# Kernel tuning notes

Measured on AMD Instinct MI355X. Metric: run time of the kernel, lower is better.

Reference implementation:

```python
import jax, jax.numpy as jnp
import numpy as np

HEADS, DHEAD = 4, 64            # TransformerConv heads / out_channels
MAX_EDGE_DIST = 1.0

def _ln(x, g, b):
    m = jnp.mean(x, -1, keepdims=True)
    v = jnp.mean((x - m) ** 2, -1, keepdims=True)
    return (x - m) * jax.lax.rsqrt(v + 1e-5) * g + b


def _embed_conv(node_feat, entity_type, adjv, mask, emb, W1, b1, g1, be1, Wh, bh, gh, beh):
    # aggr='add' message passing over dense masked adjacency. mask[b,s,t]: edge s->t.
    B, N, _ = mask.shape
    src = jnp.concatenate([node_feat, emb[entity_type]], -1)          # [B,N,F+E]
    msg = jnp.concatenate(
        [jnp.broadcast_to(src[:, :, None, :], (B, N, N, src.shape[-1])),
         adjv[..., None]], -1)                                        # [B,Ns,Nt,F+E+1]
    h = _ln(jax.nn.relu(msg @ W1 + b1), g1, be1)                      # lin1
    h = _ln(jax.nn.relu(h @ Wh + bh), gh, beh)                        # lin2[0]
    return jnp.einsum('bst,bsth->bth', mask, h)                       # sum over sources


def _tconv(x, adjv, mask, Wq, bq, Wk, bk, Wv, bv, We, Ws, bs):
    # PyG TransformerConv (beta=False, dropout=0, root_weight=True, concat=True).
    B, N, _ = x.shape
    q = (x @ Wq + bq).reshape(B, N, HEADS, DHEAD)
    k = (x @ Wk + bk).reshape(B, N, HEADS, DHEAD)
    v = (x @ Wv + bv).reshape(B, N, HEADS, DHEAD)
    we = We.reshape(HEADS, DHEAD)                                     # edge_dim=1, no bias
    scale = 1.0 / jnp.sqrt(jnp.asarray(DHEAD, x.dtype))
    # score[b,h,s,t] = q_t . (k_s + adjv[s,t]*we) * scale
    qk = jnp.einsum('bshd,bthd->bhst', k, q)
    qe = jnp.einsum('bthd,hd->bht', q, we)
    logits = (qk + adjv[:, None, :, :] * qe[:, :, None, :]) * scale
    mh = mask[:, None, :, :]                                          # [B,1,Ns,Nt]
    masked = jnp.where(mh > 0, logits, -1e30)
    mmax = jnp.max(masked, axis=2, keepdims=True)
    w = jnp.exp(masked - mmax) * mh
    den = jnp.sum(w, axis=2, keepdims=True)
    alpha = w / jnp.maximum(den, 1e-16)                               # softmax over sources per target
    out = jnp.einsum('bhst,bshd->bthd', alpha, v)
    out = out + jnp.einsum('bhst,bst->bth', alpha, adjv)[..., None] * we
    out = out.reshape(B, N, HEADS * DHEAD)
    return out + x @ Ws + bs                                          # skip (root) connection


def _forward(node_feat, entity_type, adj, agent_id, emb, W1, b1, g1, be1, Wh, bh, gh, beh,
             Wq1, bq1, Wk1, bk1, Wv1, bv1, We1, Ws1, bs1,
             Wq2, bq2, Wk2, bk2, Wv2, bv2, We2, Ws2, bs2):
    mask = ((adj > 0) & (adj < MAX_EDGE_DIST)).astype(adj.dtype)
    adjv = adj * mask
    x = _embed_conv(node_feat, entity_type, adjv, mask, emb, W1, b1, g1, be1, Wh, bh, gh, beh)
    x = jax.nn.relu(_tconv(x, adjv, mask, Wq1, bq1, Wk1, bk1, Wv1, bv1, We1, Ws1, bs1))
    x = jax.nn.relu(_tconv(x, adjv, mask, Wq2, bq2, Wk2, bk2, Wv2, bv2, We2, Ws2, bs2))
    return x[jnp.arange(x.shape[0]), agent_id]                        # gather agent node feats


def setup_inputs() -> dict:
    key = jax.random.key(0)
    ks = jax.random.split(key, 24)
    B, N, F, E, H = 32, 128, 9, 8, 128
    HD = HEADS * DHEAD
    s = 0.05
    p = lambda k, shape: (jax.random.normal(k, shape, jnp.float32) * s)
    inp = {
        'node_feat': jax.random.normal(ks[0], (B, N, F), jnp.float32),
        'entity_type': jax.random.randint(ks[1], (B, N), 0, 8),
        'adj': jax.random.uniform(ks[2], (B, N, N), jnp.float32, 0.0, 2.0),
        'agent_id': jax.random.randint(ks[3], (B,), 0, N),
        'emb': p(ks[4], (8, E)),
        'W1': p(ks[5], (F + E + 1, H)), 'b1': jnp.zeros(H), 'g1': jnp.ones(H), 'be1': jnp.zeros(H),
        'Wh': p(ks[6], (H, H)), 'bh': jnp.zeros(H), 'gh': jnp.ones(H), 'beh': jnp.zeros(H),
        'Wq1': p(ks[7], (H, HD)), 'bq1': jnp.zeros(HD),
        'Wk1': p(ks[8], (H, HD)), 'bk1': jnp.zeros(HD),
        'Wv1': p(ks[9], (H, HD)), 'bv1': jnp.zeros(HD),
        'We1': p(ks[10], (1, HD)),
        'Ws1': p(ks[11], (H, HD)), 'bs1': jnp.zeros(HD),
        'Wq2': p(ks[12], (HD, HD)), 'bq2': jnp.zeros(HD),
        'Wk2': p(ks[13], (HD, HD)), 'bk2': jnp.zeros(HD),
        'Wv2': p(ks[14], (HD, HD)), 'bv2': jnp.zeros(HD),
        'We2': p(ks[15], (1, HD)),
        'Ws2': p(ks[16], (HD, HD)), 'bs2': jnp.zeros(HD),
    }
    return inp


def reference(node_feat, entity_type, adj, agent_id, emb, W1, b1, g1, be1, Wh, bh, gh, beh,
              Wq1, bq1, Wk1, bk1, Wv1, bv1, We1, Ws1, bs1,
              Wq2, bq2, Wk2, bk2, Wv2, bv2, We2, Ws2, bs2):
    return _forward(node_feat, entity_type, adj, agent_id, emb, W1, b1, g1, be1, Wh, bh, gh, beh,
                    Wq1, bq1, Wk1, bk1, Wv1, bv1, We1, Ws1, bs1,
                    Wq2, bq2, Wk2, bk2, Wv2, bv2, We2, Ws2, bs2)
```

## Files before the change

### kernel.cpp

```cpp
#include <hip/hip_runtime.h>
#include <hip/hip_bf16.h>

typedef __hip_bfloat16 bf16;
typedef unsigned short ushort_t;
typedef unsigned char uchar_t;
typedef unsigned int uint_t;
typedef __attribute__((ext_vector_type(8))) short short8;
typedef __attribute__((ext_vector_type(4))) float fx4;
typedef __attribute__((ext_vector_type(4))) unsigned int uintx4;

#define BB 32
#define NN 128
#define FF 9
#define EE 8
#define HH 128
#define HD 256
#define NHEAD 4
#define DHEAD 64

__device__ __forceinline__ float us2f(ushort_t u) {
    return __uint_as_float(((unsigned int)u) << 16);
}
__device__ __forceinline__ ushort_t f2us_tr(float f) {
    return (ushort_t)(__float_as_uint(f) >> 16);
}
__device__ __forceinline__ short8 pack4(uint_t w0, uint_t w1, uint_t w2, uint_t w3) {
    uintx4 u = (uintx4){w0, w1, w2, w3};
    return __builtin_bit_cast(short8, u);
}
__device__ __forceinline__ void pair_split(float a, float c, uint_t& hw, uint_t& lw) {
    uint_t ua = __float_as_uint(a), uc = __float_as_uint(c);
    uint_t ka = ua & 0xffff0000u, kc = uc & 0xffff0000u;
    float la = a - __uint_as_float(ka);
    float lc = c - __uint_as_float(kc);
    hw = (ua >> 16) | kc;
    lw = (__float_as_uint(la) >> 16) | (__float_as_uint(lc) & 0xffff0000u);
}
__device__ __forceinline__ uint_t pair_hi(float a, float c) {
    return (__float_as_uint(a) >> 16) | (__float_as_uint(c) & 0xffff0000u);
}

__global__ void TransformerConvNet_85315230367963_kernel() {}

__global__ void k_sent(float* out, float val) {
    out[blockIdx.x * 256 + threadIdx.x] = val;
}

__global__ void __launch_bounds__(256) k_prep_all(
    const float* adj, float* adjvT, uchar_t* sl_s, float* sl_av, int* cnts,
    int* tmapG,
    const float* nf, const int* et, const float* emb, const float* W1,
    const float* b1, float* base, float* x0,
    const float* Wh, const float* g1, const float* be1, const float* bh,
    ushort_t* BhiG, ushort_t* BloG, float* W1s, float* cbv,
    const float* Wq1, const float* Wk1, const float* Wv1, const float* Ws1,
    ushort_t* WhA, ushort_t* WlA,
    const float* Wq2, const float* Wk2, const float* Wv2, const float* Ws2,
    ushort_t* WhB, ushort_t* WlB)
{
    __shared__ float tileF[128 * 33];
    __shared__ int   cntL[256];

    int blk = blockIdx.x;
    int tid = threadIdx.x;

    if (blk < 32) {
        int b = blk;
        int wv = tid >> 6, lane = tid & 63;
        for (int c = 0; c < 4; c++) {
            int t0c = c * 32;
#pragma unroll
            for (int pass = 0; pass < 16; pass++) {
                int s = pass * 8 + (tid >> 5);
                int tq = tid & 31;
                float a = adj[(b * NN + s) * NN + t0c + tq];
                float av = (a > 0.f && a < 1.0f) ? a : 0.f;
                tileF[s * 33 + tq] = av;
            }
            __syncthreads();
#pragma unroll
            for (int j = 0; j < 16; j++) {
                int u = wv * 16 + j;
                int tq = u >> 1, sh = u & 1;
                int t = t0c + tq;
                int s = sh * 64 + lane;
                float av = tileF[s * 33 + tq];
                adjvT[(b * NN + t) * NN + s] = av;
                unsigned long long mask = __ballot(av != 0.f);
                int key = (b * NN + t) * 2 + sh;
                if (av != 0.f) {
                    int pos = __popcll(mask & ((1ull << lane) - 1ull));
                    sl_s[key * 64 + pos] = (uchar_t)s;
                    sl_av[key * 64 + pos] = av;
                }
                if (lane == 0) {
                    int cv = (int)__popcll(mask);
                    cnts[key] = cv;
                    cntL[t * 2 + sh] = cv;
                    if (mask == 0ull) { sl_s[key * 64] = 0; sl_av[key * 64] = 0.f; }
                }
            }
            __syncthreads();
        }
        {
            int sh = tid >> 7, i = tid & 127;
            int ci = cntL[i * 2 + sh];
            int rank = 0;
            for (int j = 0; j < 128; j++) {
                int cj = cntL[j * 2 + sh];
                rank += (cj > ci) || (cj == ci && j < i);
            }
            tmapG[b * 256 + sh * 128 + rank] = i;
        }
    } else if (blk < 1056) {
        int bblk = blk - 32;
        int c = tid & 127;
#pragma unroll
        for (int rr = 0; rr < 2; rr++) {
            int bs = bblk * 4 + rr * 2 + (tid >> 7);
            int ty = et[bs];
            float acc = b1[c];
            for (int f = 0; f < FF; f++)
                acc += nf[bs * FF + f] * W1[f * HH + c];
            for (int e2 = 0; e2 < EE; e2++)
                acc += emb[ty * EE + e2] * W1[(FF + e2) * HH + c];
            base[bs * HH + c] = acc;
        }
    } else if (blk < 1312) {
        int zblk = blk - 1056;
        float4* p = (float4*)x0 + zblk * 512 + tid * 2;
        p[0] = (float4){0.f, 0.f, 0.f, 0.f};
        p[1] = (float4){0.f, 0.f, 0.f, 0.f};
    } else if (blk < 1344) {
        int n = (blk - 1312) * 4 + (tid >> 6);
        int t = tid & 63;
        int sw = 8 * (n & 15);
        float s1 = 0.f, s2 = 0.f;
#pragma unroll
        for (int kk = 0; kk < 2; kk++) {
            int k = t + kk * 64;
            float w = Wh[k * HH + n];
            float wp = g1[k] * w;
            ushort_t hb = f2us_tr(wp);
            float lo = wp - us2f(hb);
            BhiG[n * HH + (k ^ sw)] = hb;
            BloG[n * HH + (k ^ sw)] = f2us_tr(lo);
            s1 += wp;
            s2 += be1[k] * w;
        }
        for (int m = 1; m < 64; m <<= 1) {
            s1 += __shfl_xor(s1, m);
            s2 += __shfl_xor(s2, m);
        }
        if (t == 0) { W1s[n] = s1; cbv[n] = s2 + bh[n]; }
    } else if (blk < 1600) {
        int key = (blk - 1344) * 4 + (tid >> 6);
        int lane = tid & 63;
        int mat = key >> 8, n = key & 255;
        const float* W = (mat == 0) ? Wq1 : (mat == 1) ? Wk1 : (mat == 2) ? Wv1 : Ws1;
        ushort_t* hi = WhA + mat * 256 * HH;
        ushort_t* lo = WlA + mat * 256 * HH;
        int sw = 8 * (n & 15);
        for (int k = lane; k < HH; k += 64) {
            float w = W[k * HD + n];
            ushort_t hb = f2us_tr(w);
            float l = w - us2f(hb);
            hi[n * HH + (k ^ sw)] = hb;
            lo[n * HH + (k ^ sw)] = f2us_tr(l);
        }
    } else {
        int key = (blk - 1600) * 4 + (tid >> 6);
        int lane = tid & 63;
        int mat = key >> 8, n = key & 255;
        const float* W = (mat == 0) ? Wq2 : (mat == 1) ? Wk2 : (mat == 2) ? Wv2 : Ws2;
        ushort_t* hi = WhB + mat * 256 * HD;
        ushort_t* lo = WlB + mat * 256 * HD;
        int sw = 8 * (n & 15);
        for (int k = lane; k < HD; k += 64) {
            float w = W[k * HD + n];
            ushort_t hb = f2us_tr(w);
            float l = w - us2f(hb);
            hi[n * HD + (k ^ sw)] = hb;
            lo[n * HD + (k ^ sw)] = f2us_tr(l);
        }
    }
}

__global__ void __launch_bounds__(256) k_econv_mfma(
    const uchar_t* sl_s, const float* sl_av, const int* cnts, const int* tmapG,
    const float* base, const float* W1,
    const ushort_t* BhiG, const ushort_t* BloG,
    const float* W1sg, const float* cbv,
    const float* ghp, const float* behp, float* x0)
{
    __shared__ __align__(16) ushort_t PhiPlo[2 * HH * HH];
    __shared__ int tmap16[16];
    ushort_t* Phi = PhiPlo;
    ushort_t* Plo = PhiPlo + HH * HH;

    int blk = blockIdx.x;
    int b  = blk >> 4;
    int tt = (blk >> 1) & 7;
    int sh = blk & 1;
    if (b >= BB / 2) tt = 7 - tt;
    int t0 = tt * 16;
    int tid = threadIdx.x;
    int wv  = tid >> 6;
    int lane = tid & 63;
    int nl = lane & 15;
    int quad = lane >> 4;

    if (tid < 16) tmap16[tid] = tmapG[b * 256 + sh * 128 + t0 + tid];

    {
        const uint4* srcH = (const uint4*)BhiG;
        const uint4* srcL = (const uint4*)BloG;
        uint4* dstH = (uint4*)Phi;
        uint4* dstL = (uint4*)Plo;
        for (int i = tid; i < HH * HH / 8; i += 256) {
            dstH[i] = srcH[i];
            dstL[i] = srcL[i];
        }
    }

    float w17v[4][8];
#pragma unroll
    for (int st = 0; st < 4; st++) {
        const float* p = W1 + 17 * HH + quad * 8 + 32 * st;
        float4 a = *(const float4*)p;
        float4 bq = *(const float4*)(p + 4);
        w17v[st][0] = a.x;  w17v[st][1] = a.y;  w17v[st][2] = a.z;  w17v[st][3] = a.w;
        w17v[st][4] = bq.x; w17v[st][5] = bq.y; w17v[st][6] = bq.z; w17v[st][7] = bq.w;
    }

    __syncthreads();

    int myt = tmap16[nl];
    int key = ((b << 7) + myt) * 2 + sh;
    int cnt = cnts[key];
    int q = (cnt + 3) >> 2;
    int mq = q;
#pragma unroll
    for (int m = 1; m < 16; m <<= 1) mq = max(mq, __shfl_xor(mq, m));
    const uchar_t* lst_s = sl_s + key * 64;
    const float*   lst_a = sl_av + key * 64;
    int i0 = wv * q;

    fx4 acc1[8];
#pragma unroll
    for (int tile = 0; tile < 8; tile++) acc1[tile] = (fx4){0.f, 0.f, 0.f, 0.f};
    float c0 = 0.f;
    float c1 = 0.f;

    for (int i = 0; i < mq; i++) {
        int idx = i0 + i;
        bool val = (i < q) && (idx < cnt);
        int ridx = (idx < cnt) ? idx : (cnt > 0 ? cnt - 1 : 0);
        int s = lst_s[ridx];
        float avv = val ? lst_a[ridx] : 0.f;
        const float* brow = base + (b * NN + s) * HH;

        short8 Hhi[4], Hlo[4];
        float sm = 0.f, s2 = 0.f;
#pragma unroll
        for (int st = 0; st < 4; st++) {
            const float* p = brow + quad * 8 + 32 * st;
            float4 b0 = *(const float4*)p;
            float4 b1q = *(const float4*)(p + 4);
            float h[8] = {b0.x, b0.y, b0.z, b0.w, b1q.x, b1q.y, b1q.z, b1q.w};
            uint_t hw[4], lw[4];
#pragma unroll
            for (int pr = 0; pr < 4; pr++) {
                float a = fmaxf(fmaf(avv, w17v[st][2 * pr], h[2 * pr]), 0.f);
                float c = fmaxf(fmaf(avv, w17v[st][2 * pr + 1], h[2 * pr + 1]), 0.f);
                sm += a; sm += c;
                s2 = fmaf(a, a, s2);
                s2 = fmaf(c, c, s2);
                pair_split(a, c, hw[pr], lw[pr]);
            }
            Hhi[st] = pack4(hw[0], hw[1], hw[2], hw[3]);
            Hlo[st] = pack4(lw[0], lw[1], lw[2], lw[3]);
        }
        sm += __shfl_xor(sm, 16); sm += __shfl_xor(sm, 32);
        s2 += __shfl_xor(s2, 16); s2 += __shfl_xor(s2, 32);
        float m1 = sm * (1.f / 128.f);
        float r1 = rsqrtf(s2 * (1.f / 128.f) - m1 * m1 + 1e-5f);
        float nm = -m1 * r1;

        fx4 G[8];
#pragma unroll
        for (int tile = 0; tile < 8; tile++) G[tile] = (fx4){0.f, 0.f, 0.f, 0.f};
#pragma unroll
        for (int st = 0; st < 4; st++) {
            int koff = quad * 8 + 32 * st;
#pragma unroll
            for (int tile = 0; tile < 8; tile++) {
                int off = (tile * 16 + nl) * HH + (koff ^ (nl * 8));
                short8 ph = *(const short8*)(&Phi[off]);
                short8 pl = *(const short8*)(&Plo[off]);
                G[tile] = __builtin_amdgcn_mfma_f32_16x16x32_bf16(ph, Hhi[st], G[tile], 0, 0, 0);
                G[tile] = __builtin_amdgcn_mfma_f32_16x16x32_bf16(pl, Hhi[st], G[tile], 0, 0, 0);
                G[tile] = __builtin_amdgcn_mfma_f32_16x16x32_bf16(ph, Hlo[st], G[tile], 0, 0, 0);
            }
        }

        float sm2 = 0.f, ss2 = 0.f;
#pragma unroll
        for (int tile = 0; tile < 8; tile++) {
            float4 w4 = *(const float4*)(W1sg + tile * 16 + quad * 4);
            float4 c4 = *(const float4*)(cbv + tile * 16 + quad * 4);
            float wa[4] = {w4.x, w4.y, w4.z, w4.w};
            float ca[4] = {c4.x, c4.y, c4.z, c4.w};
#pragma unroll
            for (int r = 0; r < 4; r++) {
                float pre = fmaf(r1, G[tile][r], fmaf(nm, wa[r], ca[r]));
                float h2 = fmaxf(pre, 0.f);
                G[tile][r] = h2;
                sm2 += h2;
                ss2 = fmaf(h2, h2, ss2);
            }
        }
        sm2 += __shfl_xor(sm2, 16); sm2 += __shfl_xor(sm2, 32);
        ss2 += __shfl_xor(ss2, 16); ss2 += __shfl_xor(ss2, 32);
        float mean2 = sm2 * (1.f / 128.f);
        float r2 = rsqrtf(ss2 * (1.f / 128.f) - mean2 * mean2 + 1e-5f);
        float msk = val ? 1.f : 0.f;
        float mr2 = msk * r2;

#pragma unroll
        for (int tile = 0; tile < 8; tile++)
#pragma unroll
            for (int r = 0; r < 4; r++)
                acc1[tile][r] = fmaf(mr2, G[tile][r], acc1[tile][r]);
        c0 += msk;
        c1 = fmaf(mr2, mean2, c1);
    }

    __syncthreads();
    float* slab = (float*)PhiPlo;
#pragma unroll
    for (int tile = 0; tile < 8; tile++) {
        float4 g4 = *(const float4*)(ghp + tile * 16 + quad * 4);
        float4 be4 = *(const float4*)(behp + tile * 16 + quad * 4);
        float gv[4] = {g4.x, g4.y, g4.z, g4.w};
        float bv[4] = {be4.x, be4.y, be4.z, be4.w};
#pragma unroll
        for (int r = 0; r < 4; r++) {
            float xv = fmaf(gv[r], acc1[tile][r] - c1, bv[r] * c0);
            slab[(wv * 16 + nl) * 132 + tile * 16 + quad * 4 + r] = xv;
        }
    }
    __syncthreads();
    for (int e = tid; e < 16 * HH; e += 256) {
        int t = e >> 7, n = e & 127;
        float vsum = slab[t * 132 + n] + slab[(16 + t) * 132 + n]
                   + slab[(32 + t) * 132 + n] + slab[(48 + t) * 132 + n];
        atomicAdd(&x0[(b * NN + tmap16[t]) * HH + n], vsum);
    }
}

template <int IN>
__global__ void __launch_bounds__(256) k_qkvs_mfma(
    const float* x, const ushort_t* Whi, const ushort_t* Wlo,
    const float* b0, const float* b1, const float* b2, const float* b3,
    float* q, float* skipo,
    ushort_t* khi, ushort_t* klo, ushort_t* vThi, ushort_t* vTlo,
    const int* agentp)
{
    const int ST = IN / 32;
    int blk = blockIdx.x;
    int m0 = (blk >> 3) * 64;
    int nsl = blk & 7;
    int tid = threadIdx.x;
    int wv = tid >> 6;
    int lane = tid & 63;
    int nl = lane & 15;
    int quad = lane >> 4;
    int row = m0 + wv * 16 + nl;

    short8 Ahi[ST], Alo[ST];
    const float* xrow = x + (long)row * IN;
#pragma unroll
    for (int st = 0; st < ST; st++) {
        const float* p = xrow + quad * 8 + 32 * st;
        float4 a4 = *(const float4*)p;
        float4 b4 = *(const float4*)(p + 4);
        float h[8] = {a4.x, a4.y, a4.z, a4.w, b4.x, b4.y, b4.z, b4.w};
        uint_t hw[4], lw[4];
#pragma unroll
        for (int pr = 0; pr < 4; pr++)
            pair_split(h[2 * pr], h[2 * pr + 1], hw[pr], lw[pr]);
        Ahi[st] = pack4(hw[0], hw[1], hw[2], hw[3]);
        Alo[st] = pack4(lw[0], lw[1], lw[2], lw[3]);
    }

    const float* bs_[4] = {b0, b1, b2, b3};
    int rw0 = m0 + wv * 16;
    bool agset = (agentp != nullptr);
    int agrow = agset ? agentp[rw0 >> 7] : -1;
    bool havea = agset && ((agrow >> 4) == ((rw0 & 127) >> 4));

#pragma unroll
    for (int mat = 0; mat < 4; mat++) {
        if ((mat == 0 || mat == 3) && agset && !havea) continue;
        const ushort_t* Bh = Whi + (mat * 256 + nsl * 32) * IN;
        const ushort_t* Bl = Wlo + (mat * 256 + nsl * 32) * IN;
        fx4 G[2];
#pragma unroll
        for (int tile = 0; tile < 2; tile++) {
            float bc = bs_[mat][nsl * 32 + tile * 16 + nl];
            G[tile] = (fx4){bc, bc, bc, bc};
        }
#pragma unroll
        for (int st = 0; st < ST; st++) {
            int koff = quad * 8 + 32 * st;
#pragma unroll
            for (int tile = 0; tile < 2; tile++) {
                int off = (tile * 16 + nl) * IN + (koff ^ (nl * 8));
                short8 bh8 = *(const short8*)(Bh + off);
                short8 bl8 = *(const short8*)(Bl + off);
                G[tile] = __builtin_amdgcn_mfma_f32_16x16x32_bf16(Ahi[st], bh8, G[tile], 0, 0, 0);
                G[tile] = __builtin_amdgcn_mfma_f32_16x16x32_bf16(Alo[st], bh8, G[tile], 0, 0, 0);
                G[tile] = __builtin_amdgcn_mfma_f32_16x16x32_bf16(Ahi[st], bl8, G[tile], 0, 0, 0);
            }
        }
        int row0 = m0 + wv * 16 + quad * 4;
        if (mat == 0 || mat == 3) {
            float* om = (mat == 0) ? q : skipo;
#pragma unroll
            for (int tile = 0; tile < 2; tile++)
#pragma unroll
                for (int r = 0; r < 4; r++)
                    om[(row0 + r) * HD + nsl * 32 + tile * 16 + nl] = G[tile][r];
        } else if (mat == 1) {
#pragma unroll
            for (int tile = 0; tile < 2; tile++) {
                int col = nsl * 32 + tile * 16 + nl;
#pragma unroll
                for (int r = 0; r < 4; r++) {
                    float gv = G[tile][r];
                    ushort_t hb = f2us_tr(gv);
                    khi[(row0 + r) * HD + col] = hb;
                    klo[(row0 + r) * HD + col] = f2us_tr(gv - us2f(hb));
                }
            }
        } else {
            int bb = row0 >> 7;
            int s0 = row0 & 127;
#pragma unroll
            for (int tile = 0; tile < 2; tile++) {
                int col = nsl * 32 + tile * 16 + nl;
                int dg = bb * 256 + col;
                ushort4 h4, l4;
                float g0 = G[tile][0], g1 = G[tile][1], g2 = G[tile][2], g3 = G[tile][3];
                ushort_t h0 = f2us_tr(g0), h1 = f2us_tr(g1), h2 = f2us_tr(g2), h3 = f2us_tr(g3);
                h4.x = h0; h4.y = h1; h4.z = h2; h4.w = h3;
                l4.x = f2us_tr(g0 - us2f(h0));
                l4.y = f2us_tr(g1 - us2f(h1));
                l4.z = f2us_tr(g2 - us2f(h2));
                l4.w = f2us_tr(g3 - us2f(h3));
                *(ushort4*)&vThi[dg * NN + s0] = h4;
                *(ushort4*)&vTlo[dg * NN + s0] = l4;
            }
        }
    }
}

__global__ void __launch_bounds__(128) k_attn_mfma(
    const float* qb, const ushort_t* khi, const ushort_t* klo,
    const ushort_t* vThi, const ushort_t* vTlo,
    const float* adjvT, const float* We, const float* skip, float* xout,
    const int* agentp, float* outp)
{
    __shared__ float aL[16][132];
    __shared__ float qeL[16];
    __shared__ float mxL[2][16];
    __shared__ float dnL[2][16];
    __shared__ float ebL[2][16];

    int blk = blockIdx.x;
    int b, h, tt;
    if (agentp == nullptr) {
        b = blk >> 5; h = (blk >> 3) & 3; tt = blk & 7;
    } else {
        b = blk >> 2; h = blk & 3; tt = agentp[b] >> 4;
    }
    int t0 = tt * 16;
    int tid = threadIdx.x;
    int w   = tid >> 6;
    int lane = tid & 63;
    int nl = lane & 15;
    int quad = lane >> 4;

    short8 Qhi[2], Qlo[2];
    float qe = 0.f;
#pragma unroll
    for (int ks = 0; ks < 2; ks++) {
        const float* p = qb + (b * NN + t0 + nl) * HD + h * DHEAD + quad * 8 + 32 * ks;
        const float* wp = We + h * DHEAD + quad * 8 + 32 * ks;
        float4 a0 = *(const float4*)p;
        float4 a1 = *(const float4*)(p + 4);
        float4 w0 = *(const float4*)wp;
        float4 w1 = *(const float4*)(wp + 4);
        float hv[8] = {a0.x, a0.y, a0.z, a0.w, a1.x, a1.y, a1.z, a1.w};
        float wv8[8] = {w0.x, w0.y, w0.z, w0.w, w1.x, w1.y, w1.z, w1.w};
        uint_t hw[4], lw[4];
#pragma unroll
        for (int pr = 0; pr < 4; pr++) {
            float a = hv[2 * pr], c = hv[2 * pr + 1];
            qe = fmaf(a, wv8[2 * pr], qe);
            qe = fmaf(c, wv8[2 * pr + 1], qe);
            pair_split(a, c, hw[pr], lw[pr]);
        }
        Qhi[ks] = pack4(hw[0], hw[1], hw[2], hw[3]);
        Qlo[ks] = pack4(lw[0], lw[1], lw[2], lw[3]);
    }
    qe += __shfl_xor(qe, 16);
    qe += __shfl_xor(qe, 32);
    if (w == 0 && lane < 16) qeL[lane] = qe;
    __syncthreads();
    float qe_r[4];
#pragma unroll
    for (int r = 0; r < 4; r++) qe_r[r] = qeL[quad * 4 + r];
    float we_d[2];
#pragma unroll
    for (int nt2 = 0; nt2 < 2; nt2++) we_d[nt2] = We[h * DHEAD + (w * 2 + nt2) * 16 + nl];

    fx4 S[4];
#pragma unroll
    for (int st = 0; st < 4; st++) S[st] = (fx4){0.f, 0.f, 0.f, 0.f};
#pragma unroll
    for (int ks = 0; ks < 2; ks++) {
#pragma unroll
        for (int st = 0; st < 4; st++) {
            long off = (long)(b * NN + (w * 4 + st) * 16 + nl) * HD + h * DHEAD + quad * 8 + 32 * ks;
            short8 bh8 = *(const short8*)(khi + off);
            short8 bl8 = *(const short8*)(klo + off);
            S[st] = __builtin_amdgcn_mfma_f32_16x16x32_bf16(Qhi[ks], bh8, S[st], 0, 0, 0);
            S[st] = __builtin_amdgcn_mfma_f32_16x16x32_bf16(Qlo[ks], bh8, S[st], 0, 0, 0);
            S[st] = __builtin_amdgcn_mfma_f32_16x16x32_bf16(Qhi[ks], bl8, S[st], 0, 0, 0);
        }
    }

    float av[4][4];
#pragma unroll
    for (int st = 0; st < 4; st++)
#pragma unroll
        for (int r = 0; r < 4; r++)
            av[st][r] = adjvT[(b * NN + t0 + quad * 4 + r) * NN + (w * 4 + st) * 16 + nl];
#pragma unroll
    for (int st = 0; st < 4; st++)
#pragma unroll
        for (int r = 0; r < 4; r++) {
            float a = av[st][r];
            S[st][r] = (a != 0.f) ? (S[st][r] + a * qe_r[r]) * 0.125f : -1e30f;
        }

    float mxp[4];
#pragma unroll
    for (int r = 0; r < 4; r++) {
        float m = S[0][r];
#pragma unroll
        for (int st = 1; st < 4; st++) m = fmaxf(m, S[st][r]);
#pragma unroll
        for (int mm = 1; mm < 16; mm <<= 1) m = fmaxf(m, __shfl_xor(m, mm));
        mxp[r] = m;
    }
    if (nl == 0) {
#pragma unroll
        for (int r = 0; r < 4; r++) mxL[w][quad * 4 + r] = mxp[r];
    }
    __syncthreads();
    float mx[4];
#pragma unroll
    for (int r = 0; r < 4; r++)
        mx[r] = fmaxf(mxL[0][quad * 4 + r], mxL[1][quad * 4 + r]);

    float dnp[4] = {0.f, 0.f, 0.f, 0.f}, ebp[4] = {0.f, 0.f, 0.f, 0.f};
#pragma unroll
    for (int st = 0; st < 4; st++)
#pragma unroll
        for (int r = 0; r < 4; r++) {
            float e = (av[st][r] != 0.f) ? __expf(S[st][r] - mx[r]) : 0.f;
            S[st][r] = e;
            dnp[r] += e;
            ebp[r] = fmaf(e, av[st][r], ebp[r]);
        }
#pragma unroll
    for (int r = 0; r < 4; r++) {
#pragma unroll
        for (int mm = 1; mm < 16; mm <<= 1) {
            dnp[r] += __shfl_xor(dnp[r], mm);
            ebp[r] += __shfl_xor(ebp[r], mm);
        }
    }
    if (nl == 0) {
#pragma unroll
        for (int r = 0; r < 4; r++) {
            dnL[w][quad * 4 + r] = dnp[r];
            ebL[w][quad * 4 + r] = ebp[r];
        }
    }
    __syncthreads();
    float rden[4], beta[4];
#pragma unroll
    for (int r = 0; r < 4; r++) {
        int row = quad * 4 + r;
        float d = dnL[0][row] + dnL[1][row];
        rden[r] = 1.f / fmaxf(d, 1e-16f);
        beta[r] = (ebL[0][row] + ebL[1][row]) * rden[r];
    }

#pragma unroll
    for (int st = 0; st < 4; st++)
#pragma unroll
        for (int r = 0; r < 4; r++)
            aL[quad * 4 + r][(w * 4 + st) * 16 + nl] = S[st][r] * rden[r];
    __syncthreads();

    short8 Ah[4];
#pragma unroll
    for (int ks = 0; ks < 4; ks++) {
        const float* p = &aL[nl][quad * 8 + 32 * ks];
        float4 a0 = *(const float4*)p;
        float4 a1 = *(const float4*)(p + 4);
        float hv[8] = {a0.x, a0.y, a0.z, a0.w, a1.x, a1.y, a1.z, a1.w};
        uint_t ww[4];
#pragma unroll
        for (int pr = 0; pr < 4; pr++) ww[pr] = pair_hi(hv[2 * pr], hv[2 * pr + 1]);
        Ah[ks] = pack4(ww[0], ww[1], ww[2], ww[3]);
    }

    fx4 G[2];
#pragma unroll
    for (int nt2 = 0; nt2 < 2; nt2++) {
        fx4 g;
#pragma unroll
        for (int r = 0; r < 4; r++) g[r] = beta[r] * we_d[nt2];
        G[nt2] = g;
    }
#pragma unroll
    for (int ks = 0; ks < 4; ks++) {
#pragma unroll
        for (int nt2 = 0; nt2 < 2; nt2++) {
            long dg = (long)(b * 256 + h * DHEAD + (w * 2 + nt2) * 16 + nl);
            const short8 vh = *(const short8*)(vThi + dg * NN + quad * 8 + 32 * ks);
            const short8 vl = *(const short8*)(vTlo + dg * NN + quad * 8 + 32 * ks);
            G[nt2] = __builtin_amdgcn_mfma_f32_16x16x32_bf16(Ah[ks], vh, G[nt2], 0, 0, 0);
            G[nt2] = __builtin_amdgcn_mfma_f32_16x16x32_bf16(Ah[ks], vl, G[nt2], 0, 0, 0);
        }
    }

    if (agentp == nullptr) {
#pragma unroll
        for (int nt2 = 0; nt2 < 2; nt2++)
#pragma unroll
            for (int r = 0; r < 4; r++) {
                int gi = (b * NN + t0 + quad * 4 + r) * HD + h * DHEAD + (w * 2 + nt2) * 16 + nl;
                xout[gi] = fmaxf(G[nt2][r] + skip[gi], 0.f);
            }
    } else {
        int ag = agentp[b];
#pragma unroll
        for (int nt2 = 0; nt2 < 2; nt2++)
#pragma unroll
            for (int r = 0; r < 4; r++) {
                int t = t0 + quad * 4 + r;
                if (t == ag) {
                    int d = h * DHEAD + (w * 2 + nt2) * 16 + nl;
                    int gi = (b * NN + t) * HD + d;
                    outp[b * HD + d] = fmaxf(G[nt2][r] + skip[gi], 0.f);
                }
            }
    }
}

extern "C" void kernel_launch(void* const* d_in, const int* in_sizes, int n_in,
                              void* d_out, int out_size, void* d_ws, size_t ws_size,
                              hipStream_t stream) {
    float* out = (float*)d_out;
    (void)hipGetLastError();

    bool ok = (n_in == 31) && in_sizes[0] == BB * NN * FF && in_sizes[2] == BB * NN * NN
              && in_sizes[5] == (FF + EE + 1) * HH && in_sizes[13] == HH * HD
              && in_sizes[22] == HD * HD && out_size == BB * HD;
    if (!ok) { k_sent<<<32, 256, 0, stream>>>(out, -30000.f); return; }

    const size_t WS_NEED = (size_t)8912896 * 4;
    if (ws_size < WS_NEED) { k_sent<<<32, 256, 0, stream>>>(out, -20000.f); return; }

    const float* nf    = (const float*)d_in[0];
    const int*   et    = (const int*)d_in[1];
    const float* adj   = (const float*)d_in[2];
    const int*   agent = (const int*)d_in[3];
    const float* emb   = (const float*)d_in[4];
    const float* W1    = (const float*)d_in[5];
    const float* b1    = (const float*)d_in[6];
    const float* g1    = (const float*)d_in[7];
    const float* be1   = (const float*)d_in[8];
    const float* Wh    = (const float*)d_in[9];
    const float* bh    = (const float*)d_in[10];
    const float* gh    = (const float*)d_in[11];
    const float* beh   = (const float*)d_in[12];
    const float* Wq1   = (const float*)d_in[13];
    const float* bq1   = (const float*)d_in[14];
    const float* Wk1   = (const float*)d_in[15];
    const float* bk1   = (const float*)d_in[16];
    const float* Wv1   = (const float*)d_in[17];
    const float* bv1   = (const float*)d_in[18];
    const float* We1   = (const float*)d_in[19];
    const float* Ws1   = (const float*)d_in[20];
    const float* bs1   = (const float*)d_in[21];
    const float* Wq2   = (const float*)d_in[22];
    const float* bq2   = (const float*)d_in[23];
    const float* Wk2   = (const float*)d_in[24];
    const float* bk2   = (const float*)d_in[25];
    const float* Wv2   = (const float*)d_in[26];
    const float* bv2   = (const float*)d_in[27];
    const float* We2   = (const float*)d_in[28];
    const float* Ws2   = (const float*)d_in[29];
    const float* bs2   = (const float*)d_in[30];

    float* ws   = (float*)d_ws;
    float* slav = ws;
    float* base = ws + 524288;
    float* x0   = base + BB * NN * HH;
    float* q    = x0 + BB * NN * HH;
    float* kreg = q + BB * NN * HD;
    float* vreg = kreg + BB * NN * HD;
    float* skip = vreg + BB * NN * HD;
    float* areg = skip + BB * NN * HD;
    float* x1   = areg + BB * NN * HD;
    float* x2   = x1 + BB * NN * HD;

    ushort_t* BhiG = (ushort_t*)q;
    ushort_t* BloG = BhiG + HH * HH;
    float*    W1sW = q + 16384;
    float*    cbW  = q + 16512;
    int*      cnts = (int*)(q + 17024);
    int*      tmapG = (int*)(q + 25216);

    ushort_t* khi  = (ushort_t*)kreg;
    ushort_t* klo  = khi + BB * NN * HD;
    ushort_t* vThi = (ushort_t*)vreg;
    ushort_t* vTlo = vThi + BB * NN * HD;

    ushort_t* WhA = (ushort_t*)areg;
    ushort_t* WlA = WhA + 4 * 256 * HH;
    ushort_t* WhB = WlA + 4 * 256 * HH;
    ushort_t* WlB = WhB + 4 * 256 * HD;
    float* adjvT  = areg + 393216;
    uchar_t* sl_s = (uchar_t*)(areg + 917504);

    int fail = 0;
    hipError_t e;
#define CHK(stage) do { e = hipGetLastError(); if (e != hipSuccess && fail == 0) fail = (stage); } while (0)

    k_prep_all<<<1856, 256, 0, stream>>>(
        adj, adjvT, sl_s, slav, cnts, tmapG,
        nf, et, emb, W1, b1, base, x0,
        Wh, g1, be1, bh, BhiG, BloG, W1sW, cbW,
        Wq1, Wk1, Wv1, Ws1, WhA, WlA,
        Wq2, Wk2, Wv2, Ws2, WhB, WlB);                                               CHK(1);

    k_econv_mfma<<<512, 256, 0, stream>>>(sl_s, slav, cnts, tmapG, base, W1,
                                          BhiG, BloG, W1sW, cbW, gh, beh, x0);       CHK(2);

    k_qkvs_mfma<HH><<<512, 256, 0, stream>>>(x0, WhA, WlA, bq1, bk1, bv1, bs1,
                                             q, skip, khi, klo, vThi, vTlo,
                                             nullptr);                               CHK(3);
    k_attn_mfma<<<1024, 128, 0, stream>>>(q, khi, klo, vThi, vTlo, adjvT, We1,
                                          skip, x1, nullptr, nullptr);               CHK(4);

    k_qkvs_mfma<HD><<<512, 256, 0, stream>>>(x1, WhB, WlB, bq2, bk2, bv2, bs2,
                                             q, skip, khi, klo, vThi, vTlo,
                                             agent);                                 CHK(5);
    k_attn_mfma<<<128, 128, 0, stream>>>(q, khi, klo, vThi, vTlo, adjvT, We2,
                                         skip, x2, agent, out);                      CHK(6);
#undef CHK

    if (fail != 0)
        k_sent<<<32, 256, 0, stream>>>(out, -(1000.f + 500.f * (float)fail));
}
```

Baseline: 253.5 us.

## Split adjacency prep across more blocks and widen attention blocks to four waves

The adjacency preprocessing that ran in 32 blocks, each looping over four target chunks, now runs in 128 blocks, one per batch and chunk. A separate set of 32 blocks recomputes per-target counts straight from adj to build the sorted target map. The attention kernel moves from 2 to 4 waves per block, so each wave handles half as many source tiles and one output column tile, and the cross-wave reductions now combine four partials. The aim is more parallelism and shorter serial chains per wave, at the cost of redundant adj reads for the counts and more shared-memory reduction traffic.

```diff
diff --git a/kernel.cpp b/kernel.cpp
--- a/kernel.cpp
+++ b/kernel.cpp
@@ -59,61 +59,72 @@
     ushort_t* WhB, ushort_t* WlB)
 {
     __shared__ float tileF[128 * 33];
-    __shared__ int   cntL[256];
+    __shared__ int   cntP[512];
+    __shared__ int   combL[256];
 
     int blk = blockIdx.x;
     int tid = threadIdx.x;
 
-    if (blk < 32) {
-        int b = blk;
+    if (blk < 128) {
+        int b = blk >> 2, c = blk & 3;
         int wv = tid >> 6, lane = tid & 63;
-        for (int c = 0; c < 4; c++) {
-            int t0c = c * 32;
-#pragma unroll
-            for (int pass = 0; pass < 16; pass++) {
-                int s = pass * 8 + (tid >> 5);
-                int tq = tid & 31;
-                float a = adj[(b * NN + s) * NN + t0c + tq];
-                float av = (a > 0.f && a < 1.0f) ? a : 0.f;
-                tileF[s * 33 + tq] = av;
-            }
-            __syncthreads();
-#pragma unroll
-            for (int j = 0; j < 16; j++) {
-                int u = wv * 16 + j;
-                int tq = u >> 1, sh = u & 1;
-                int t = t0c + tq;
-                int s = sh * 64 + lane;
-                float av = tileF[s * 33 + tq];
-                adjvT[(b * NN + t) * NN + s] = av;
-                unsigned long long mask = __ballot(av != 0.f);
-                int key = (b * NN + t) * 2 + sh;
-                if (av != 0.f) {
-                    int pos = __popcll(mask & ((1ull << lane) - 1ull));
-                    sl_s[key * 64 + pos] = (uchar_t)s;
-                    sl_av[key * 64 + pos] = av;
-                }
-                if (lane == 0) {
-                    int cv = (int)__popcll(mask);
-                    cnts[key] = cv;
-                    cntL[t * 2 + sh] = cv;
-                    if (mask == 0ull) { sl_s[key * 64] = 0; sl_av[key * 64] = 0.f; }
-                }
-            }
-            __syncthreads();
-        }
-        {
-            int sh = tid >> 7, i = tid & 127;
-            int ci = cntL[i * 2 + sh];
-            int rank = 0;
-            for (int j = 0; j < 128; j++) {
-                int cj = cntL[j * 2 + sh];
-                rank += (cj > ci) || (cj == ci && j < i);
-            }
-            tmapG[b * 256 + sh * 128 + rank] = i;
-        }
-    } else if (blk < 1056) {
-        int bblk = blk - 32;
+        int t0c = c * 32;
+#pragma unroll
+        for (int pass = 0; pass < 16; pass++) {
+            int s = pass * 8 + (tid >> 5);
+            int tq = tid & 31;
+            float a = adj[(b * NN + s) * NN + t0c + tq];
+            float av = (a > 0.f && a < 1.0f) ? a : 0.f;
+            tileF[s * 33 + tq] = av;
+        }
+        __syncthreads();
+#pragma unroll
+        for (int j = 0; j < 16; j++) {
+            int u = wv * 16 + j;
+            int tq = u >> 1, sh = u & 1;
+            int t = t0c + tq;
+            int s = sh * 64 + lane;
+            float av = tileF[s * 33 + tq];
+            adjvT[(b * NN + t) * NN + s] = av;
+            unsigned long long mask = __ballot(av != 0.f);
+            int key = (b * NN + t) * 2 + sh;
+            if (av != 0.f) {
+                int pos = __popcll(mask & ((1ull << lane) - 1ull));
+                sl_s[key * 64 + pos] = (uchar_t)s;
+                sl_av[key * 64 + pos] = av;
+            }
+            if (lane == 0) {
+                cnts[key] = (int)__popcll(mask);
+                if (mask == 0ull) { sl_s[key * 64] = 0; sl_av[key * 64] = 0.f; }
+            }
+        }
+    } else if (blk < 160) {
+        int b = blk - 128;
+        int t = tid & 127, p = tid >> 7;
+        int c0 = 0, c1 = 0;
+        for (int k = 0; k < 32; k++) {
+            float a = adj[(b * NN + (2 * k + p)) * NN + t];
+            c0 += (a > 0.f && a < 1.0f) ? 1 : 0;
+        }
+        for (int k = 32; k < 64; k++) {
+            float a = adj[(b * NN + (2 * k + p)) * NN + t];
+            c1 += (a > 0.f && a < 1.0f) ? 1 : 0;
+        }
+        cntP[p * 256 + t * 2 + 0] = c0;
+        cntP[p * 256 + t * 2 + 1] = c1;
+        __syncthreads();
+        int sh = tid >> 7, i = tid & 127;
+        int ci = cntP[0 * 256 + i * 2 + sh] + cntP[1 * 256 + i * 2 + sh];
+        combL[i * 2 + sh] = ci;
+        __syncthreads();
+        int rank = 0;
+        for (int j = 0; j < 128; j++) {
+            int cj = combL[j * 2 + sh];
+            rank += (cj > ci) || (cj == ci && j < i);
+        }
+        tmapG[b * 256 + sh * 128 + rank] = i;
+    } else if (blk < 1184) {
+        int bblk = blk - 160;
         int c = tid & 127;
 #pragma unroll
         for (int rr = 0; rr < 2; rr++) {
@@ -126,13 +137,13 @@
                 acc += emb[ty * EE + e2] * W1[(FF + e2) * HH + c];
             base[bs * HH + c] = acc;
         }
-    } else if (blk < 1312) {
-        int zblk = blk - 1056;
+    } else if (blk < 1440) {
+        int zblk = blk - 1184;
         float4* p = (float4*)x0 + zblk * 512 + tid * 2;
         p[0] = (float4){0.f, 0.f, 0.f, 0.f};
         p[1] = (float4){0.f, 0.f, 0.f, 0.f};
-    } else if (blk < 1344) {
-        int n = (blk - 1312) * 4 + (tid >> 6);
+    } else if (blk < 1472) {
+        int n = (blk - 1440) * 4 + (tid >> 6);
         int t = tid & 63;
         int sw = 8 * (n & 15);
         float s1 = 0.f, s2 = 0.f;
@@ -153,8 +164,8 @@
             s2 += __shfl_xor(s2, m);
         }
         if (t == 0) { W1s[n] = s1; cbv[n] = s2 + bh[n]; }
-    } else if (blk < 1600) {
-        int key = (blk - 1344) * 4 + (tid >> 6);
+    } else if (blk < 1728) {
+        int key = (blk - 1472) * 4 + (tid >> 6);
         int lane = tid & 63;
         int mat = key >> 8, n = key & 255;
         const float* W = (mat == 0) ? Wq1 : (mat == 1) ? Wk1 : (mat == 2) ? Wv1 : Ws1;
@@ -169,7 +180,7 @@
             lo[n * HH + (k ^ sw)] = f2us_tr(l);
         }
     } else {
-        int key = (blk - 1600) * 4 + (tid >> 6);
+        int key = (blk - 1728) * 4 + (tid >> 6);
         int lane = tid & 63;
         int mat = key >> 8, n = key & 255;
         const float* W = (mat == 0) ? Wq2 : (mat == 1) ? Wk2 : (mat == 2) ? Wv2 : Ws2;
@@ -466,7 +477,7 @@
     }
 }
 
-__global__ void __launch_bounds__(128) k_attn_mfma(
+__global__ void __launch_bounds__(256) k_attn_mfma(
     const float* qb, const ushort_t* khi, const ushort_t* klo,
     const ushort_t* vThi, const ushort_t* vTlo,
     const float* adjvT, const float* We, const float* skip, float* xout,
@@ -474,9 +485,9 @@
 {
     __shared__ float aL[16][132];
     __shared__ float qeL[16];
-    __shared__ float mxL[2][16];
-    __shared__ float dnL[2][16];
-    __shared__ float ebL[2][16];
+    __shared__ float mxL[4][16];
+    __shared__ float dnL[4][16];
+    __shared__ float ebL[4][16];
 
     int blk = blockIdx.x;
     int b, h, tt;
@@ -522,18 +533,16 @@
     float qe_r[4];
 #pragma unroll
     for (int r = 0; r < 4; r++) qe_r[r] = qeL[quad * 4 + r];
-    float we_d[2];
-#pragma unroll
-    for (int nt2 = 0; nt2 < 2; nt2++) we_d[nt2] = We[h * DHEAD + (w * 2 + nt2) * 16 + nl];
-
-    fx4 S[4];
-#pragma unroll
-    for (int st = 0; st < 4; st++) S[st] = (fx4){0.f, 0.f, 0.f, 0.f};
+    float we_dv = We[h * DHEAD + w * 16 + nl];
+
+    fx4 S[2];
+#pragma unroll
+    for (int st = 0; st < 2; st++) S[st] = (fx4){0.f, 0.f, 0.f, 0.f};
 #pragma unroll
     for (int ks = 0; ks < 2; ks++) {
 #pragma unroll
-        for (int st = 0; st < 4; st++) {
-            long off = (long)(b * NN + (w * 4 + st) * 16 + nl) * HD + h * DHEAD + quad * 8 + 32 * ks;
+        for (int st = 0; st < 2; st++) {
+            long off = (long)(b * NN + (w * 2 + st) * 16 + nl) * HD + h * DHEAD + quad * 8 + 32 * ks;
             short8 bh8 = *(const short8*)(khi + off);
             short8 bl8 = *(const short8*)(klo + off);
             S[st] = __builtin_amdgcn_mfma_f32_16x16x32_bf16(Qhi[ks], bh8, S[st], 0, 0, 0);
@@ -542,14 +551,14 @@
         }
     }
 
-    float av[4][4];
-#pragma unroll
-    for (int st = 0; st < 4; st++)
+    float av[2][4];
+#pragma unroll
+    for (int st = 0; st < 2; st++)
 #pragma unroll
         for (int r = 0; r < 4; r++)
-            av[st][r] = adjvT[(b * NN + t0 + quad * 4 + r) * NN + (w * 4 + st) * 16 + nl];
-#pragma unroll
-    for (int st = 0; st < 4; st++)
+            av[st][r] = adjvT[(b * NN + t0 + quad * 4 + r) * NN + (w * 2 + st) * 16 + nl];
+#pragma unroll
+    for (int st = 0; st < 2; st++)
 #pragma unroll
         for (int r = 0; r < 4; r++) {
             float a = av[st][r];
@@ -559,9 +568,7 @@
     float mxp[4];
 #pragma unroll
     for (int r = 0; r < 4; r++) {
-        float m = S[0][r];
-#pragma unroll
-        for (int st = 1; st < 4; st++) m = fmaxf(m, S[st][r]);
+        float m = fmaxf(S[0][r], S[1][r]);
 #pragma unroll
         for (int mm = 1; mm < 16; mm <<= 1) m = fmaxf(m, __shfl_xor(m, mm));
         mxp[r] = m;
@@ -573,12 +580,15 @@
     __syncthreads();
     float mx[4];
 #pragma unroll
-    for (int r = 0; r < 4; r++)
-        mx[r] = fmaxf(mxL[0][quad * 4 + r], mxL[1][quad * 4 + r]);
+    for (int r = 0; r < 4; r++) {
+        int row = quad * 4 + r;
+        mx[r] = fmaxf(fmaxf(mxL[0][row], mxL[1][row]),
+                      fmaxf(mxL[2][row], mxL[3][row]));
+    }
 
     float dnp[4] = {0.f, 0.f, 0.f, 0.f}, ebp[4] = {0.f, 0.f, 0.f, 0.f};
 #pragma unroll
-    for (int st = 0; st < 4; st++)
+    for (int st = 0; st < 2; st++)
 #pragma unroll
         for (int r = 0; r < 4; r++) {
             float e = (av[st][r] != 0.f) ? __expf(S[st][r] - mx[r]) : 0.f;
@@ -606,16 +616,16 @@
 #pragma unroll
     for (int r = 0; r < 4; r++) {
         int row = quad * 4 + r;
-        float d = dnL[0][row] + dnL[1][row];
+        float d = ((dnL[0][row] + dnL[1][row]) + dnL[2][row]) + dnL[3][row];
         rden[r] = 1.f / fmaxf(d, 1e-16f);
-        beta[r] = (ebL[0][row] + ebL[1][row]) * rden[r];
-    }
-
-#pragma unroll
-    for (int st = 0; st < 4; st++)
+        beta[r] = (((ebL[0][row] + ebL[1][row]) + ebL[2][row]) + ebL[3][row]) * rden[r];
+    }
+
+#pragma unroll
+    for (int st = 0; st < 2; st++)
 #pragma unroll
         for (int r = 0; r < 4; r++)
-            aL[quad * 4 + r][(w * 4 + st) * 16 + nl] = S[st][r] * rden[r];
+            aL[quad * 4 + r][(w * 2 + st) * 16 + nl] = S[st][r] * rden[r];
     __syncthreads();
 
     short8 Ah[4];
@@ -631,47 +641,39 @@
         Ah[ks] = pack4(ww[0], ww[1], ww[2], ww[3]);
     }
 
-    fx4 G[2];
-#pragma unroll
-    for (int nt2 = 0; nt2 < 2; nt2++) {
-        fx4 g;
-#pragma unroll
-        for (int r = 0; r < 4; r++) g[r] = beta[r] * we_d[nt2];
-        G[nt2] = g;
-    }
-#pragma unroll
-    for (int ks = 0; ks < 4; ks++) {
-#pragma unroll
-        for (int nt2 = 0; nt2 < 2; nt2++) {
-            long dg = (long)(b * 256 + h * DHEAD + (w * 2 + nt2) * 16 + nl);
-            const short8 vh = *(const short8*)(vThi + dg * NN + quad * 8 + 32 * ks);
-            const short8 vl = *(const short8*)(vTlo + dg * NN + quad * 8 + 32 * ks);
-            G[nt2] = __builtin_amdgcn_mfma_f32_16x16x32_bf16(Ah[ks], vh, G[nt2], 0, 0, 0);
-            G[nt2] = __builtin_amdgcn_mfma_f32_16x16x32_bf16(Ah[ks], vl, G[nt2], 0, 0, 0);
+    fx4 G;
+#pragma unroll
+    for (int r = 0; r < 4; r++) G[r] = beta[r] * we_dv;
+    {
+        long dg = (long)(b * 256 + h * DHEAD + w * 16 + nl);
+        const ushort_t* vhB = vThi + dg * NN;
+        const ushort_t* vlB = vTlo + dg * NN;
+#pragma unroll
+        for (int ks = 0; ks < 4; ks++) {
+            const short8 vh = *(const short8*)(vhB + quad * 8 + 32 * ks);
+            const short8 vl = *(const short8*)(vlB + quad * 8 + 32 * ks);
+            G = __builtin_amdgcn_mfma_f32_16x16x32_bf16(Ah[ks], vh, G, 0, 0, 0);
+            G = __builtin_amdgcn_mfma_f32_16x16x32_bf16(Ah[ks], vl, G, 0, 0, 0);
         }
     }
 
     if (agentp == nullptr) {
 #pragma unroll
-        for (int nt2 = 0; nt2 < 2; nt2++)
-#pragma unroll
-            for (int r = 0; r < 4; r++) {
-                int gi = (b * NN + t0 + quad * 4 + r) * HD + h * DHEAD + (w * 2 + nt2) * 16 + nl;
-                xout[gi] = fmaxf(G[nt2][r] + skip[gi], 0.f);
-            }
+        for (int r = 0; r < 4; r++) {
+            int gi = (b * NN + t0 + quad * 4 + r) * HD + h * DHEAD + w * 16 + nl;
+            xout[gi] = fmaxf(G[r] + skip[gi], 0.f);
+        }
     } else {
         int ag = agentp[b];
 #pragma unroll
-        for (int nt2 = 0; nt2 < 2; nt2++)
-#pragma unroll
-            for (int r = 0; r < 4; r++) {
-                int t = t0 + quad * 4 + r;
-                if (t == ag) {
-                    int d = h * DHEAD + (w * 2 + nt2) * 16 + nl;
-                    int gi = (b * NN + t) * HD + d;
-                    outp[b * HD + d] = fmaxf(G[nt2][r] + skip[gi], 0.f);
-                }
-            }
+        for (int r = 0; r < 4; r++) {
+            int t = t0 + quad * 4 + r;
+            if (t == ag) {
+                int d = h * DHEAD + w * 16 + nl;
+                int gi = (b * NN + t) * HD + d;
+                outp[b * HD + d] = fmaxf(G[r] + skip[gi], 0.f);
+            }
+        }
     }
 }
 
@@ -756,7 +758,7 @@
     hipError_t e;
 #define CHK(stage) do { e = hipGetLastError(); if (e != hipSuccess && fail == 0) fail = (stage); } while (0)
 
-    k_prep_all<<<1856, 256, 0, stream>>>(
+    k_prep_all<<<1984, 256, 0, stream>>>(
         adj, adjvT, sl_s, slav, cnts, tmapG,
         nf, et, emb, W1, b1, base, x0,
         Wh, g1, be1, bh, BhiG, BloG, W1sW, cbW,
@@ -769,13 +771,13 @@
     k_qkvs_mfma<HH><<<512, 256, 0, stream>>>(x0, WhA, WlA, bq1, bk1, bv1, bs1,
                                              q, skip, khi, klo, vThi, vTlo,
                                              nullptr);                               CHK(3);
-    k_attn_mfma<<<1024, 128, 0, stream>>>(q, khi, klo, vThi, vTlo, adjvT, We1,
+    k_attn_mfma<<<1024, 256, 0, stream>>>(q, khi, klo, vThi, vTlo, adjvT, We1,
                                           skip, x1, nullptr, nullptr);               CHK(4);
 
     k_qkvs_mfma<HD><<<512, 256, 0, stream>>>(x1, WhB, WlB, bq2, bk2, bv2, bs2,
                                              q, skip, khi, klo, vThi, vTlo,
                                              agent);                                 CHK(5);
-    k_attn_mfma<<<128, 128, 0, stream>>>(q, khi, klo, vThi, vTlo, adjvT, We2,
+    k_attn_mfma<<<128, 256, 0, stream>>>(q, khi, klo, vThi, vTlo, adjvT, We2,
                                          skip, x2, agent, out);                      CHK(6);
 #undef CHK
 
```

Measured after the change: 245.3 us. -3.2%, faster.
